# Performance work log

Hardware: AMD Instinct MI355X
Metric: run time of the kernel (lower is better)

Reference implementation:

```python
import jax, jax.numpy as jnp
import numpy as np

B, H, W, L, R = 8, 32, 32, 6, 384
NH = 6                      # num_heads
NE = L * R                  # n_embd = 2304
HID = 4 * NE                # tree-MLP hidden
M = sum(4 ** i for i in range(L))  # 1365 unique tree nodes
EPS = 1e-5


def build_node_id_map(h, w, l):
    # (h,w,level) -> unique node id; level k patches are 2^k x 2^k blocks
    ids = np.zeros((h, w, l), np.int32)
    off = 0
    for k in range(l):
        ws = w >> k
        hh = (np.arange(h) >> k)[:, None]
        ww = (np.arange(w) >> k)[None, :]
        ids[:, :, k] = off + hh * ws + ww
        off += (h >> k) * ws
    assert off == M
    return ids

_IDS = jnp.asarray(build_node_id_map(H, W, L).reshape(-1))  # (H*W*L,)


def layernorm(x, w, b):
    mu = jnp.mean(x, axis=-1, keepdims=True)
    var = jnp.mean(jnp.square(x - mu), axis=-1, keepdims=True)
    return (x - mu) * jax.lax.rsqrt(var + EPS) * w + b


def setup_inputs() -> dict:
    key = jax.random.key(0)
    ks = jax.random.split(key, 12)
    s = 0.02
    return {
        "x": jax.random.normal(ks[0], (B, H, W, L, R), jnp.float32),
        "ln1_w": jnp.ones((R,), jnp.float32), "ln1_b": jnp.zeros((R,), jnp.float32),
        "ln2_w": jnp.ones((R,), jnp.float32), "ln2_b": jnp.zeros((R,), jnp.float32),
        "wq": s * jax.random.normal(ks[1], (R, R), jnp.float32), "bq": jnp.zeros((R,), jnp.float32),
        "wk": s * jax.random.normal(ks[2], (R, R), jnp.float32), "bk": jnp.zeros((R,), jnp.float32),
        "wv": s * jax.random.normal(ks[3], (R, R), jnp.float32), "bv": jnp.zeros((R,), jnp.float32),
        "wo": s * jax.random.normal(ks[4], (R, R), jnp.float32), "bo": jnp.zeros((R,), jnp.float32),
        "w1": s * jax.random.normal(ks[5], (NE, HID), jnp.float32), "b1": jnp.zeros((HID,), jnp.float32),
        "w2": s * jax.random.normal(ks[6], (HID, NE), jnp.float32), "b2": jnp.zeros((NE,), jnp.float32),
    }


def reference(x, ln1_w, ln1_b, ln2_w, ln2_b, wq, bq, wk, bk, wv, bv, wo, bo, w1, b1, w2, b2):
    dh = R // NH
    # (1) LN per node
    x_ln = layernorm(x, ln1_w, ln1_b)
    # (2) unify duplicates -> (B, M, R) via segment mean over node ids
    xf = x_ln.reshape(B, H * W * L, R)
    counts = jnp.zeros((M,), x.dtype).at[_IDS].add(1.0)
    uniq = jnp.zeros((B, M, R), x.dtype).at[:, _IDS].add(xf) / counts[None, :, None]
    # (3) multi-head self-attention over the M unique tree nodes
    q = (uniq @ wq + bq).reshape(B, M, NH, dh)
    k = (uniq @ wk + bk).reshape(B, M, NH, dh)
    v = (uniq @ wv + bv).reshape(B, M, NH, dh)
    logits = jnp.einsum("bmhd,bnhd->bhmn", q, k) * (1.0 / jnp.sqrt(jnp.asarray(dh, x.dtype)))
    attn = jax.nn.softmax(logits, axis=-1)
    o = jnp.einsum("bhmn,bnhd->bmhd", attn, v).reshape(B, M, R)
    attn_out = o @ wo + bo
    # (4) scatter back to (B,H,W,L,R)
    x_attn = attn_out[:, _IDS].reshape(B, H, W, L, R)
    # (5) residual (dropout is identity in eval)
    x_res = x + x_attn
    # (6) LN -> tree MLP over full level stack at each (h,w)
    x_ln2 = layernorm(x_res, ln2_w, ln2_b)
    flat = x_ln2.reshape(B, H, W, NE)
    h1 = jax.nn.gelu(flat @ w1 + b1)
    mlp_out = (h1 @ w2 + b2).reshape(B, H, W, L, R)
    # (7) residual
    return x_res + mlp_out
```

## Files before the change

kernel.cpp:

```cpp
#include <hip/hip_runtime.h>
#include <cstddef>

#define B_    8
#define H_    32
#define W_    32
#define L_    6
#define R_    384
#define NH_   6
#define DH_   64
#define M_    1365
#define MPAD_ 1408
#define NE_   2304
#define HID_  9216
#define NROW_ 49152
#define BMR_  10920

typedef __bf16 bf16x8 __attribute__((ext_vector_type(8)));
typedef float  f32x4  __attribute__((ext_vector_type(4)));
typedef unsigned short us;

__device__ __forceinline__ unsigned short f2b(float f){
  unsigned u = __float_as_uint(f);
  u = (u + 0x7FFFu + ((u >> 16) & 1u)) >> 16;
  return (unsigned short)u;
}

__device__ __forceinline__ void gload16(const unsigned short* g, unsigned short* l){
  __builtin_amdgcn_global_load_lds(
      (const __attribute__((address_space(1))) unsigned int*)g,
      (__attribute__((address_space(3))) unsigned int*)l,
      16, 0, 0);
}

__device__ __forceinline__ float wsum(float s){
  #pragma unroll
  for (int o = 32; o > 0; o >>= 1) s += __shfl_xor(s, o, 64);
  return s;
}

__device__ __forceinline__ float rmax16(float v){
  v = fmaxf(v, __shfl_xor(v, 1, 64));
  v = fmaxf(v, __shfl_xor(v, 2, 64));
  v = fmaxf(v, __shfl_xor(v, 4, 64));
  v = fmaxf(v, __shfl_xor(v, 8, 64));
  return v;
}
__device__ __forceinline__ float rsum16(float v){
  v += __shfl_xor(v, 1, 64);
  v += __shfl_xor(v, 2, 64);
  v += __shfl_xor(v, 4, 64);
  v += __shfl_xor(v, 8, 64);
  return v;
}

__device__ __forceinline__ float gelu_fast(float x){
  float t = fmaf(0.07135482f * x, x * x, 1.5957691216f * x);
  return x / (1.0f + __expf(-t));
}

__global__ __launch_bounds__(256) void k_ln1_scatter(
    const float* __restrict__ x, const float* __restrict__ lw,
    const float* __restrict__ lb, float* __restrict__ uniq){
  int row  = blockIdx.x * 4 + (threadIdx.x >> 6);
  int lane = threadIdx.x & 63;
  int l  = row % 6;
  int hw = (row / 6) & 1023;
  int b  = row / 6144;
  int h = hw >> 5, w = hw & 31;
  const float* xr = x + (size_t)row * R_;
  float v[6]; float s = 0.f;
  #pragma unroll
  for (int i = 0; i < 6; i++){ v[i] = xr[lane + i*64]; s += v[i]; }
  s = wsum(s);
  float mu = s * (1.f/384.f);
  float qq = 0.f;
  #pragma unroll
  for (int i = 0; i < 6; i++){ float d = v[i]-mu; qq += d*d; }
  qq = wsum(qq);
  float rs = rsqrtf(qq * (1.f/384.f) + 1e-5f);
  int off = (4096 - (4096 >> (2*l))) / 3;
  int id  = off + (h >> l) * (32 >> l) + (w >> l);
  float invc = 1.f / (float)(1 << (2*l));
  float* ur = uniq + ((size_t)b * M_ + id) * R_;
  #pragma unroll
  for (int i = 0; i < 6; i++){
    int r = lane + i*64;
    float ln = (v[i]-mu)*rs*lw[r] + lb[r];
    atomicAdd(&ur[r], ln * invc);
  }
}

__global__ void k_cvt(const float* __restrict__ src, unsigned short* __restrict__ dst, int n){
  int i = blockIdx.x * 256 + threadIdx.x;
  if (i < n) dst[i] = f2b(src[i]);
}

__global__ void k_tcvt(const float* __restrict__ src, unsigned short* __restrict__ dst,
                       int K, int N){
  __shared__ float t[32][33];
  int n0 = blockIdx.x * 32, k0 = blockIdx.y * 32;
  int tx = threadIdx.x, ty = threadIdx.y;
  #pragma unroll
  for (int i = 0; i < 4; i++)
    t[ty + i*8][tx] = src[(size_t)(k0 + ty + i*8) * N + n0 + tx];
  __syncthreads();
  #pragma unroll
  for (int i = 0; i < 4; i++)
    dst[(size_t)(n0 + ty + i*8) * K + k0 + tx] = f2b(t[tx][ty + i*8]);
}

template<int EPI>
__global__ __launch_bounds__(256) void k_gemm(
    const unsigned short* __restrict__ A,
    const unsigned short* __restrict__ Bt,
    const float* __restrict__ bias,
    void* __restrict__ Cout,
    const float* __restrict__ res,
    void* __restrict__ aux1, void* __restrict__ aux2,
    int Mtot, int N, int K){
  __shared__ unsigned short As[128*64];
  __shared__ unsigned short Bs[128*64];
  int m0 = blockIdx.x * 128, n0 = blockIdx.y * 128;
  int tid  = threadIdx.x;
  int wv   = tid >> 6, lane = tid & 63;
  int quad = lane >> 4, l16 = lane & 15;
  int wm = (wv >> 1) * 64, wn = (wv & 1) * 64;
  int lr = lane >> 3;
  int lc = (lane & 7) * 8;
  f32x4 acc[4][4];
  #pragma unroll
  for (int a = 0; a < 4; a++)
    #pragma unroll
    for (int bidx = 0; bidx < 4; bidx++) acc[a][bidx] = 0.f;

  for (int k0 = 0; k0 < K; k0 += 64){
    #pragma unroll
    for (int j = 0; j < 4; j++){
      int c = wv*4 + j;
      int rowa = c*8 + lr;
      int gm = m0 + rowa; if (gm >= Mtot) gm = Mtot - 1;
      gload16(A + (size_t)gm * K + k0 + lc, &As[c*512]);
      int gn = n0 + rowa;
      gload16(Bt + (size_t)gn * K + k0 + lc, &Bs[c*512]);
    }
    asm volatile("s_waitcnt vmcnt(0)" ::: "memory");
    __syncthreads();
    #pragma unroll
    for (int ko = 0; ko < 2; ko++){
      bf16x8 af[4], bfr[4];
      #pragma unroll
      for (int t = 0; t < 4; t++){
        af[t]  = *(const bf16x8*)(&As[(wm + t*16 + l16)*64 + ko*32 + quad*8]);
        bfr[t] = *(const bf16x8*)(&Bs[(wn + t*16 + l16)*64 + ko*32 + quad*8]);
      }
      #pragma unroll
      for (int mt = 0; mt < 4; mt++)
        #pragma unroll
        for (int nt = 0; nt < 4; nt++)
          acc[mt][nt] = __builtin_amdgcn_mfma_f32_16x16x32_bf16(
              af[mt], bfr[nt], acc[mt][nt], 0, 0, 0);
    }
    __syncthreads();
  }
  #pragma unroll
  for (int mt = 0; mt < 4; mt++){
    #pragma unroll
    for (int i = 0; i < 4; i++){
      int row = m0 + wm + mt*16 + quad*4 + i;
      if (row >= Mtot) continue;
      #pragma unroll
      for (int nt = 0; nt < 4; nt++){
        int col = n0 + wn + nt*16 + l16;
        size_t idx = (size_t)row * N + col;
        float vv = acc[mt][nt][i] + bias[col];
        if (EPI == 5){
          int bb = row / M_;
          int mm = row - bb * M_;
          if (col < 384){
            ((unsigned short*)Cout)[(size_t)row * R_ + col] = f2b(vv);
          } else if (col < 768){
            ((unsigned short*)aux1)[(size_t)row * R_ + col - 384] = f2b(vv);
          } else {
            int c2 = col - 768;
            int hh = c2 >> 6, dd = c2 & 63;
            ((unsigned short*)aux2)[(((size_t)(bb*NH_ + hh))*DH_ + dd)*MPAD_ + mm] = f2b(vv);
          }
        } else {
          ((float*)Cout)[idx] = vv;
        }
      }
    }
  }
}


__device__ __forceinline__ void stage_half(const unsigned short* __restrict__ g,
                                           unsigned short* l, int K){
  int tid = threadIdx.x;
  int w  = tid >> 6;
  int ln = tid & 63;
  int rw = ln >> 3;
  int cs = ((ln & 7) ^ rw) * 8;
  gload16(g + (size_t)(w*16 + rw)     * K + cs, l + (w*16)*64);
  gload16(g + (size_t)(w*16 + 8 + rw) * K + cs, l + (w*16 + 8)*64);
}

__device__ __forceinline__ bf16x8 ldsfrag(const unsigned short* base, int row, int ko, int quad){
  int g = ((ko << 2) + quad) ^ (row & 7);
  return *(const bf16x8*)(base + row*64 + g*8);
}

#define SB0()  __builtin_amdgcn_sched_barrier(0)
#define MFMA16(A8, B8, C4) __builtin_amdgcn_mfma_f32_16x16x32_bf16(A8, B8, C4, 0, 0, 0)

#define PHASE(P, STAGE_STMT, TAIL_STMT)                                          \
  { bf16x8 aL0 = ldsfrag(curA, wr*128 + (2*(P))*16   + l16, 0, quad);            \
    bf16x8 aH0 = ldsfrag(curA, wr*128 + (2*(P))*16   + l16, 1, quad);            \
    bf16x8 aL1 = ldsfrag(curA, wr*128 + (2*(P)+1)*16 + l16, 0, quad);            \
    bf16x8 aH1 = ldsfrag(curA, wr*128 + (2*(P)+1)*16 + l16, 1, quad);            \
    STAGE_STMT;                                                                  \
    SB0();                                                                       \
    __builtin_amdgcn_s_barrier();                                                \
    asm volatile("s_waitcnt lgkmcnt(0)" ::: "memory");                           \
    SB0();                                                                       \
    __builtin_amdgcn_s_setprio(1);                                               \
    _Pragma("unroll")                                                            \
    for (int nt = 0; nt < 4; nt++)                                               \
      acc[2*(P)][nt]   = MFMA16(aL0, bfr[nt][0], acc[2*(P)][nt]);                \
    _Pragma("unroll")                                                            \
    for (int nt = 0; nt < 4; nt++)                                               \
      acc[2*(P)+1][nt] = MFMA16(aL1, bfr[nt][0], acc[2*(P)+1][nt]);              \
    _Pragma("unroll")                                                            \
    for (int nt = 0; nt < 4; nt++)                                               \
      acc[2*(P)][nt]   = MFMA16(aH0, bfr[nt][1], acc[2*(P)][nt]);                \
    _Pragma("unroll")                                                            \
    for (int nt = 0; nt < 4; nt++)                                               \
      acc[2*(P)+1][nt] = MFMA16(aH1, bfr[nt][1], acc[2*(P)+1][nt]);              \
    __builtin_amdgcn_s_setprio(0);                                               \
    TAIL_STMT;                                                                   \
    SB0();                                                                       \
    __builtin_amdgcn_s_barrier();                                                \
    SB0(); }

#define KTILE(CURBUF)                                                            \
  { us* curA = &lds8[CURBUF][0];                                                 \
    us* curB = curA + 16384;                                                     \
    us* nxtA = &lds8[(CURBUF) ^ 1][0];                                           \
    bool st1 = (t + 1 < NT), st2 = (t + 2 < NT);                                 \
    const us* An = Ab + (size_t)(t + 1) * 64;                                    \
    const us* Bn = Bb + (size_t)(t + 2) * 64;                                    \
    bf16x8 bfr[4][2];                                                            \
    _Pragma("unroll")                                                            \
    for (int nt = 0; nt < 4; nt++){                                              \
      bfr[nt][0] = ldsfrag(curB, wc*64 + nt*16 + l16, 0, quad);                  \
      bfr[nt][1] = ldsfrag(curB, wc*64 + nt*16 + l16, 1, quad);                  \
    }                                                                            \
    PHASE(0, { if (st1) stage_half(An,          nxtA,        Kfull); }, {});     \
    PHASE(1, { if (st1) stage_half(An + 128*KS, nxtA + 8192, Kfull); }, {});     \
    PHASE(2, { if (st2) stage_half(Bn,          curB,        Kfull); }, {});     \
    PHASE(3, { if (st2) stage_half(Bn + 128*KS, curB + 8192, Kfull); },          \
             { if (st1){                                                         \
                 if (st2) asm volatile("s_waitcnt vmcnt(4)" ::: "memory");       \
                 else     asm volatile("s_waitcnt vmcnt(0)" ::: "memory");       \
               } });                                                             \
    ++t; }

template<int EPI>
__global__ __launch_bounds__(512, 2) void k_gemm8(
    const unsigned short* __restrict__ A,
    const unsigned short* __restrict__ Bt,
    const float* __restrict__ bias,
    void* __restrict__ Cout,
    int Mtot, int N, int Kfull, int kLen){
  __shared__ unsigned short lds8[2][32768];

  int m0 = blockIdx.x * 256, n0 = blockIdx.y * 256;
  int k0 = blockIdx.z * kLen;
  int NT = kLen >> 6;
  const size_t KS = (size_t)Kfull;
  const us* Ab = A  + (size_t)m0 * KS + k0;
  const us* Bb = Bt + (size_t)n0 * KS + k0;
  int tid = threadIdx.x, wv = tid >> 6, lane = tid & 63;
  int quad = lane >> 4, l16 = lane & 15;
  int wr = wv >> 2, wc = wv & 3;

  f32x4 acc[8][4];
  #pragma unroll
  for (int a = 0; a < 8; a++)
    #pragma unroll
    for (int b = 0; b < 4; b++) acc[a][b] = 0.f;

  stage_half(Bb,               &lds8[0][16384],        Kfull);
  stage_half(Bb + 128*KS,      &lds8[0][16384 + 8192], Kfull);
  stage_half(Ab,               &lds8[0][0],            Kfull);
  stage_half(Ab + 128*KS,      &lds8[0][8192],         Kfull);
  if (NT > 1){
    stage_half(Bb + 64,             &lds8[1][16384],        Kfull);
    stage_half(Bb + 128*KS + 64,    &lds8[1][16384 + 8192], Kfull);
    asm volatile("s_waitcnt vmcnt(4)" ::: "memory");
  } else {
    asm volatile("s_waitcnt vmcnt(0)" ::: "memory");
  }
  __builtin_amdgcn_s_barrier();
  SB0();

  int t = 0;
  while (t < NT){
    KTILE(0);
    KTILE(1);
  }

  #pragma unroll
  for (int mt = 0; mt < 8; mt++){
    #pragma unroll
    for (int i = 0; i < 4; i++){
      int row = m0 + wr*128 + mt*16 + quad*4 + i;
      #pragma unroll
      for (int nt = 0; nt < 4; nt++){
        int col = n0 + wc*64 + nt*16 + l16;
        size_t idx = (size_t)row * N + col;
        float vv = acc[mt][nt][i];
        if (EPI == 1){
          ((unsigned short*)Cout)[idx] = f2b(gelu_fast(vv + bias[col]));
        } else {
          atomicAdd(&((float*)Cout)[idx], vv);
        }
      }
    }
  }
}

__global__ __launch_bounds__(256) void k_attn(
    const unsigned short* __restrict__ qb, const unsigned short* __restrict__ kb,
    const unsigned short* __restrict__ vtb, unsigned short* __restrict__ ob){
  __shared__ unsigned short Ks[64][64];
  __shared__ unsigned short Vt[64][64];
  __shared__ unsigned short Ps[4][16][64];
  int qt = blockIdx.x, bh = blockIdx.y;
  int b = bh / NH_, h = bh % NH_;
  int tid = threadIdx.x, wv = tid >> 6, lane = tid & 63;
  int quad = lane >> 4, l16 = lane & 15;

  int qm = qt*64 + wv*16 + l16;
  const unsigned short* qrow = qb + (size_t)(b*M_ + qm)*R_ + h*DH_;
  bf16x8 aq0 = *(const bf16x8*)(qrow + quad*8);
  bf16x8 aq1 = *(const bf16x8*)(qrow + 32 + quad*8);

  f32x4 oacc[4];
  #pragma unroll
  for (int db = 0; db < 4; db++) oacc[db] = 0.f;
  float mi[4], li[4];
  #pragma unroll
  for (int i = 0; i < 4; i++){ mi[i] = -1e30f; li[i] = 0.f; }

  for (int kt = 0; kt < 22; kt++){
    #pragma unroll
    for (int i = 0; i < 2; i++){
      int c = tid + i*256;
      int rowa = c >> 3, colc = (c & 7) * 8;
      *(uint4*)(&Ks[rowa][colc]) =
        *(const uint4*)(kb + (size_t)(b*M_ + kt*64 + rowa)*R_ + h*DH_ + colc);
      *(uint4*)(&Vt[rowa][colc]) =
        *(const uint4*)(vtb + ((size_t)bh*DH_ + rowa)*MPAD_ + kt*64 + colc);
    }
    __syncthreads();

    f32x4 s[4];
    #pragma unroll
    for (int nb = 0; nb < 4; nb++){
      s[nb] = 0.f;
      bf16x8 bk0 = *(const bf16x8*)(&Ks[nb*16 + l16][quad*8]);
      bf16x8 bk1 = *(const bf16x8*)(&Ks[nb*16 + l16][32 + quad*8]);
      s[nb] = __builtin_amdgcn_mfma_f32_16x16x32_bf16(aq0, bk0, s[nb], 0, 0, 0);
      s[nb] = __builtin_amdgcn_mfma_f32_16x16x32_bf16(aq1, bk1, s[nb], 0, 0, 0);
    }

    #pragma unroll
    for (int i = 0; i < 4; i++){
      float val[4];
      float mx = -1e30f;
      #pragma unroll
      for (int nb = 0; nb < 4; nb++){
        int gc = kt*64 + nb*16 + l16;
        val[nb] = (gc < M_) ? s[nb][i] * 0.125f : -1e30f;
        mx = fmaxf(mx, val[nb]);
      }
      mx = rmax16(mx);
      float mnew = fmaxf(mi[i], mx);
      float alpha = __expf(mi[i] - mnew);
      float rs = 0.f;
      #pragma unroll
      for (int nb = 0; nb < 4; nb++){
        float p = __expf(val[nb] - mnew);
        rs += p;
        Ps[wv][quad*4 + i][nb*16 + l16] = f2b(p);
      }
      rs = rsum16(rs);
      li[i] = li[i]*alpha + rs;
      mi[i] = mnew;
      #pragma unroll
      for (int db = 0; db < 4; db++) oacc[db][i] *= alpha;
    }

    #pragma unroll
    for (int ko = 0; ko < 2; ko++){
      bf16x8 ap = *(const bf16x8*)(&Ps[wv][l16][ko*32 + quad*8]);
      #pragma unroll
      for (int db = 0; db < 4; db++){
        bf16x8 bv = *(const bf16x8*)(&Vt[db*16 + l16][ko*32 + quad*8]);
        oacc[db] = __builtin_amdgcn_mfma_f32_16x16x32_bf16(ap, bv, oacc[db], 0, 0, 0);
      }
    }
    __syncthreads();
  }

  #pragma unroll
  for (int i = 0; i < 4; i++){
    int gm = qt*64 + wv*16 + quad*4 + i;
    if (gm < M_){
      float il = 1.f / li[i];
      #pragma unroll
      for (int db = 0; db < 4; db++)
        ob[(size_t)(b*M_ + gm)*R_ + h*DH_ + db*16 + l16] = f2b(oacc[db][i] * il);
    }
  }
}

__global__ __launch_bounds__(256) void k_scatter_ln2(
    const float* __restrict__ x, const float* __restrict__ attn,
    const float* __restrict__ lw, const float* __restrict__ lb,
    const float* __restrict__ b2,
    float* __restrict__ xres, unsigned short* __restrict__ flatb){
  int row  = blockIdx.x * 4 + (threadIdx.x >> 6);
  int lane = threadIdx.x & 63;
  int l  = row % 6;
  int hw = (row / 6) & 1023;
  int b  = row / 6144;
  int h = hw >> 5, w = hw & 31;
  int off = (4096 - (4096 >> (2*l))) / 3;
  int id  = off + (h >> l) * (32 >> l) + (w >> l);
  const float* ar = attn + ((size_t)b * M_ + id) * R_;
  const float* xr = x + (size_t)row * R_;
  float* orow = xres + (size_t)row * R_;
  float vv[6]; float s = 0.f;
  #pragma unroll
  for (int i = 0; i < 6; i++){
    int r = lane + i*64;
    float t = xr[r] + ar[r];
    vv[i] = t; s += t;
    orow[r] = t + b2[l*R_ + r];
  }
  s = wsum(s);
  float mu = s * (1.f/384.f);
  float qq = 0.f;
  #pragma unroll
  for (int i = 0; i < 6; i++){ float d = vv[i]-mu; qq += d*d; }
  qq = wsum(qq);
  float rs = rsqrtf(qq * (1.f/384.f) + 1e-5f);
  unsigned short* fr = flatb + (size_t)row * R_;
  #pragma unroll
  for (int i = 0; i < 6; i++){
    int r = lane + i*64;
    fr[r] = f2b((vv[i]-mu)*rs*lw[r] + lb[r]);
  }
}

extern "C" void kernel_launch(void* const* d_in, const int* in_sizes, int n_in,
                              void* d_out, int out_size, void* d_ws, size_t ws_size,
                              hipStream_t stream){
  const float* x    = (const float*)d_in[0];
  const float* ln1w = (const float*)d_in[1];
  const float* ln1b = (const float*)d_in[2];
  const float* ln2w = (const float*)d_in[3];
  const float* ln2b = (const float*)d_in[4];
  const float* wq   = (const float*)d_in[5];
  const float* bq   = (const float*)d_in[6];
  const float* wk   = (const float*)d_in[7];
  const float* bk   = (const float*)d_in[8];
  const float* wvv  = (const float*)d_in[9];
  const float* bv   = (const float*)d_in[10];
  const float* wo   = (const float*)d_in[11];
  const float* bo   = (const float*)d_in[12];
  const float* w1   = (const float*)d_in[13];
  const float* b1   = (const float*)d_in[14];
  const float* w2   = (const float*)d_in[15];
  const float* b2   = (const float*)d_in[16];
  float* out = (float*)d_out;

  char* ws = (char*)d_ws;
  unsigned short* h1b = (unsigned short*)ws;
  unsigned short* qb  = (unsigned short*)ws;
  unsigned short* kb  = qb + (size_t)BMR_ * R_;
  unsigned short* vtb = kb + (size_t)BMR_ * R_;
  unsigned short* ob  = vtb + (size_t)B_ * NH_ * DH_ * MPAD_;
  float* attn_o = (float*)(ob + (size_t)BMR_ * R_);
  size_t regA = ((size_t)8192 * HID_ * 2 + 255) & ~(size_t)255;
  char* p = ws + regA;
  float* uniqf = (float*)p;                   p += (size_t)BMR_ * R_ * 4;
  unsigned short* uniqb = (unsigned short*)p; p += (size_t)BMR_ * R_ * 2;
  unsigned short* wqkvt = (unsigned short*)p; p += (size_t)3 * R_ * R_ * 2;
  unsigned short* wot = (unsigned short*)p;   p += (size_t)R_ * R_ * 2;
  unsigned short* w1t = (unsigned short*)p;   p += (size_t)NE_ * HID_ * 2;
  unsigned short* w2t = (unsigned short*)p;   p += (size_t)NE_ * HID_ * 2;
  unsigned short* flatb = (unsigned short*)p; p += (size_t)NROW_ * R_ * 2;
  float* bqkv = (float*)p;                    p += (size_t)3 * R_ * 4;

  hipMemsetAsync(uniqf, 0, (size_t)BMR_ * R_ * 4, stream);
  hipMemsetAsync(vtb, 0, (size_t)B_ * NH_ * DH_ * MPAD_ * 2, stream);
  hipMemcpyAsync(bqkv,        bq, R_*4, hipMemcpyDeviceToDevice, stream);
  hipMemcpyAsync(bqkv + R_,   bk, R_*4, hipMemcpyDeviceToDevice, stream);
  hipMemcpyAsync(bqkv + 2*R_, bv, R_*4, hipMemcpyDeviceToDevice, stream);

  k_ln1_scatter<<<NROW_/4, 256, 0, stream>>>(x, ln1w, ln1b, uniqf);
  k_cvt<<<(BMR_*R_ + 255)/256, 256, 0, stream>>>(uniqf, uniqb, BMR_*R_);

  dim3 tb(32, 8);
  k_tcvt<<<dim3(R_/32, R_/32), tb, 0, stream>>>(wq, wqkvt, R_, R_);
  k_tcvt<<<dim3(R_/32, R_/32), tb, 0, stream>>>(wk, wqkvt + (size_t)R_*R_, R_, R_);
  k_tcvt<<<dim3(R_/32, R_/32), tb, 0, stream>>>(wvv, wqkvt + (size_t)2*R_*R_, R_, R_);
  k_tcvt<<<dim3(R_/32, R_/32), tb, 0, stream>>>(wo, wot, R_, R_);
  k_tcvt<<<dim3(HID_/32, NE_/32), tb, 0, stream>>>(w1, w1t, NE_, HID_);
  k_tcvt<<<dim3(NE_/32, HID_/32), tb, 0, stream>>>(w2, w2t, HID_, NE_);

  k_gemm<5><<<dim3(86, 9), 256, 0, stream>>>(uniqb, wqkvt, bqkv, qb, nullptr,
                                             kb, vtb, BMR_, 3*R_, R_);

  k_attn<<<dim3(22, 48), 256, 0, stream>>>(qb, kb, vtb, ob);

  k_gemm<0><<<dim3(86, 3), 256, 0, stream>>>(ob, wot, bo, attn_o, nullptr,
                                             nullptr, nullptr, BMR_, R_, R_);

  k_scatter_ln2<<<NROW_/4, 256, 0, stream>>>(x, attn_o, ln2w, ln2b, b2, out, flatb);

  k_gemm8<1><<<dim3(32, 36), 512, 0, stream>>>(flatb, w1t, b1, h1b,
                                               8192, HID_, NE_, NE_);
  k_gemm8<3><<<dim3(32, 9, 2), 512, 0, stream>>>(h1b, w2t, nullptr, out,
                                                 8192, NE_, HID_, HID_/2);
}
```

Before: 1.453 ms.

## Restructure GEMM k-tile schedule to double-buffer A fragments and cut barriers

Replaces the four barrier-separated phases per k-tile with a software-pipelined schedule. A-fragment LDS reads for the next row pair are issued while the current MFMA cluster runs, using partial lgkmcnt waits, and only two s_barriers are kept per tile instead of eight. Global-to-LDS staging of the next A and B tiles is grouped into two bursts. This targets barrier stalls and LDS-read latency at the cost of more live fragment registers and trickier synchronisation: the B staging into curB now depends on a single mid-tile barrier to avoid racing with other waves still reading it.

```diff
diff --git a/kernel.cpp b/kernel.cpp
--- a/kernel.cpp
+++ b/kernel.cpp
@@ -213,34 +213,28 @@
 #define SB0()  __builtin_amdgcn_sched_barrier(0)
 #define MFMA16(A8, B8, C4) __builtin_amdgcn_mfma_f32_16x16x32_bf16(A8, B8, C4, 0, 0, 0)
 
-#define PHASE(P, STAGE_STMT, TAIL_STMT)                                          \
-  { bf16x8 aL0 = ldsfrag(curA, wr*128 + (2*(P))*16   + l16, 0, quad);            \
-    bf16x8 aH0 = ldsfrag(curA, wr*128 + (2*(P))*16   + l16, 1, quad);            \
-    bf16x8 aL1 = ldsfrag(curA, wr*128 + (2*(P)+1)*16 + l16, 0, quad);            \
-    bf16x8 aH1 = ldsfrag(curA, wr*128 + (2*(P)+1)*16 + l16, 1, quad);            \
-    STAGE_STMT;                                                                  \
-    SB0();                                                                       \
-    __builtin_amdgcn_s_barrier();                                                \
-    asm volatile("s_waitcnt lgkmcnt(0)" ::: "memory");                           \
-    SB0();                                                                       \
-    __builtin_amdgcn_s_setprio(1);                                               \
+#define CL2(I0, AF)                                                              \
+  { __builtin_amdgcn_s_setprio(1);                                              \
     _Pragma("unroll")                                                            \
     for (int nt = 0; nt < 4; nt++)                                               \
-      acc[2*(P)][nt]   = MFMA16(aL0, bfr[nt][0], acc[2*(P)][nt]);                \
+      acc[I0][nt]   = MFMA16(AF[0][0], bfr[nt][0], acc[I0][nt]);                 \
     _Pragma("unroll")                                                            \
     for (int nt = 0; nt < 4; nt++)                                               \
-      acc[2*(P)+1][nt] = MFMA16(aL1, bfr[nt][0], acc[2*(P)+1][nt]);              \
+      acc[I0+1][nt] = MFMA16(AF[1][0], bfr[nt][0], acc[I0+1][nt]);               \
     _Pragma("unroll")                                                            \
     for (int nt = 0; nt < 4; nt++)                                               \
-      acc[2*(P)][nt]   = MFMA16(aH0, bfr[nt][1], acc[2*(P)][nt]);                \
+      acc[I0][nt]   = MFMA16(AF[0][1], bfr[nt][1], acc[I0][nt]);                 \
     _Pragma("unroll")                                                            \
     for (int nt = 0; nt < 4; nt++)                                               \
-      acc[2*(P)+1][nt] = MFMA16(aH1, bfr[nt][1], acc[2*(P)+1][nt]);              \
-    __builtin_amdgcn_s_setprio(0);                                               \
-    TAIL_STMT;                                                                   \
-    SB0();                                                                       \
-    __builtin_amdgcn_s_barrier();                                                \
-    SB0(); }
+      acc[I0+1][nt] = MFMA16(AF[1][1], bfr[nt][1], acc[I0+1][nt]);               \
+    __builtin_amdgcn_s_setprio(0); }
+
+#define RDA(DST, RBASE)                                                          \
+  _Pragma("unroll")                                                              \
+  for (int r = 0; r < 2; r++){                                                   \
+    DST[r][0] = ldsfrag(curA, wr*128 + ((RBASE)+r)*16 + l16, 0, quad);           \
+    DST[r][1] = ldsfrag(curA, wr*128 + ((RBASE)+r)*16 + l16, 1, quad);           \
+  }
 
 #define KTILE(CURBUF)                                                            \
   { us* curA = &lds8[CURBUF][0];                                                 \
@@ -249,20 +243,48 @@
     bool st1 = (t + 1 < NT), st2 = (t + 2 < NT);                                 \
     const us* An = Ab + (size_t)(t + 1) * 64;                                    \
     const us* Bn = Bb + (size_t)(t + 2) * 64;                                    \
-    bf16x8 bfr[4][2];                                                            \
+    bf16x8 bfr[4][2], a0[2][2], a1[2][2];                                        \
+        \
     _Pragma("unroll")                                                            \
     for (int nt = 0; nt < 4; nt++){                                              \
       bfr[nt][0] = ldsfrag(curB, wc*64 + nt*16 + l16, 0, quad);                  \
       bfr[nt][1] = ldsfrag(curB, wc*64 + nt*16 + l16, 1, quad);                  \
     }                                                                            \
-    PHASE(0, { if (st1) stage_half(An,          nxtA,        Kfull); }, {});     \
-    PHASE(1, { if (st1) stage_half(An + 128*KS, nxtA + 8192, Kfull); }, {});     \
-    PHASE(2, { if (st2) stage_half(Bn,          curB,        Kfull); }, {});     \
-    PHASE(3, { if (st2) stage_half(Bn + 128*KS, curB + 8192, Kfull); },          \
-             { if (st1){                                                         \
-                 if (st2) asm volatile("s_waitcnt vmcnt(4)" ::: "memory");       \
-                 else     asm volatile("s_waitcnt vmcnt(0)" ::: "memory");       \
-               } });                                                             \
+    SB0();                                                                       \
+    RDA(a0, 0); SB0();                                                           \
+    RDA(a1, 2); SB0();                                                           \
+    if (st1){ stage_half(An,          nxtA,        Kfull);                       \
+              stage_half(An + 128*KS, nxtA + 8192, Kfull); }                     \
+    SB0();                                                                       \
+    asm volatile("s_waitcnt lgkmcnt(4)" ::: "memory");    \
+    SB0();                                                                       \
+    CL2(0, a0);                                                                  \
+    SB0();                                                                       \
+    RDA(a0, 4); SB0();                                   \
+    asm volatile("s_waitcnt lgkmcnt(4)" ::: "memory");              \
+    SB0();                                                                       \
+    CL2(2, a1);                                                                  \
+    SB0();                                                                       \
+    __builtin_amdgcn_s_barrier();                      \
+    SB0();                                                                       \
+    if (st2){ stage_half(Bn,          curB,        Kfull);                       \
+              stage_half(Bn + 128*KS, curB + 8192, Kfull); }                     \
+    SB0();                                                                       \
+    RDA(a1, 6); SB0();                                   \
+    asm volatile("s_waitcnt lgkmcnt(4)" ::: "memory");        \
+    SB0();                                                                       \
+    CL2(4, a0);                                                                  \
+    SB0();                                                                       \
+    asm volatile("s_waitcnt lgkmcnt(0)" ::: "memory");        \
+    SB0();                                                                       \
+    CL2(6, a1);                                                                  \
+    SB0();                                                                       \
+    if (st1){                                                                    \
+      if (st2) asm volatile("s_waitcnt vmcnt(4)" ::: "memory");                  \
+      else     asm volatile("s_waitcnt vmcnt(0)" ::: "memory");                  \
+    }                                                                            \
+    __builtin_amdgcn_s_barrier();                                                \
+    SB0();                                                                       \
     ++t; }
 
 template<int EPI>
```

After: 1.420 ms. 1.02x faster.

## Replace 256x256 eight-wave MLP GEMM with 128x128 four-wave triple-buffer-style kernel

Applied to the files above, without the earlier changes.

The two large MLP GEMMs move from a 256x256 tile with 512 threads and a four-phase interleaved staging schedule to a 128x128 tile with 256 threads. Each K-step loads all fragments, barriers, issues the t+2 prefetch into the current buffer, runs 32 MFMAs, then waits. The smaller tile quadruples the grid and lowers LDS and registers per block, which helps occupancy and load balance. In exchange, arithmetic intensity per tile drops, global and L2 traffic roughly doubles, and the simpler schedule overlaps loads and compute less finely.

```diff
diff --git a/kernel.cpp b/kernel.cpp
--- a/kernel.cpp
+++ b/kernel.cpp
@@ -194,15 +194,16 @@
 }
 
 
-__device__ __forceinline__ void stage_half(const unsigned short* __restrict__ g,
-                                           unsigned short* l, int K){
+__device__ __forceinline__ void stage_tileO(const unsigned short* __restrict__ g,
+                                            unsigned short* l, int K){
   int tid = threadIdx.x;
   int w  = tid >> 6;
   int ln = tid & 63;
   int rw = ln >> 3;
   int cs = ((ln & 7) ^ rw) * 8;
-  gload16(g + (size_t)(w*16 + rw)     * K + cs, l + (w*16)*64);
-  gload16(g + (size_t)(w*16 + 8 + rw) * K + cs, l + (w*16 + 8)*64);
+  #pragma unroll
+  for (int k = 0; k < 4; k++)
+    gload16(g + (size_t)(w*32 + k*8 + rw) * K + cs, l + (w*32 + k*8)*64);
 }
 
 __device__ __forceinline__ bf16x8 ldsfrag(const unsigned short* base, int row, int ko, int quad){
@@ -213,91 +214,76 @@
 #define SB0()  __builtin_amdgcn_sched_barrier(0)
 #define MFMA16(A8, B8, C4) __builtin_amdgcn_mfma_f32_16x16x32_bf16(A8, B8, C4, 0, 0, 0)
 
-#define PHASE(P, STAGE_STMT, TAIL_STMT)                                          \
-  { bf16x8 aL0 = ldsfrag(curA, wr*128 + (2*(P))*16   + l16, 0, quad);            \
-    bf16x8 aH0 = ldsfrag(curA, wr*128 + (2*(P))*16   + l16, 1, quad);            \
-    bf16x8 aL1 = ldsfrag(curA, wr*128 + (2*(P)+1)*16 + l16, 0, quad);            \
-    bf16x8 aH1 = ldsfrag(curA, wr*128 + (2*(P)+1)*16 + l16, 1, quad);            \
-    STAGE_STMT;                                                                  \
-    SB0();                                                                       \
-    __builtin_amdgcn_s_barrier();                                                \
-    asm volatile("s_waitcnt lgkmcnt(0)" ::: "memory");                           \
-    SB0();                                                                       \
-    __builtin_amdgcn_s_setprio(1);                                               \
+#define KTILEO(CURBUF)                                                           \
+  { const us* curA = &ldsO[CURBUF][0];                                           \
+    const us* curB = curA + 8192;                                                \
+    bool st2 = (t + 2 < NT), st1 = (t + 1 < NT);                                 \
+    bf16x8 af[4][2], bfr[4][2];                                                  \
     _Pragma("unroll")                                                            \
-    for (int nt = 0; nt < 4; nt++)                                               \
-      acc[2*(P)][nt]   = MFMA16(aL0, bfr[nt][0], acc[2*(P)][nt]);                \
-    _Pragma("unroll")                                                            \
-    for (int nt = 0; nt < 4; nt++)                                               \
-      acc[2*(P)+1][nt] = MFMA16(aL1, bfr[nt][0], acc[2*(P)+1][nt]);              \
-    _Pragma("unroll")                                                            \
-    for (int nt = 0; nt < 4; nt++)                                               \
-      acc[2*(P)][nt]   = MFMA16(aH0, bfr[nt][1], acc[2*(P)][nt]);                \
-    _Pragma("unroll")                                                            \
-    for (int nt = 0; nt < 4; nt++)                                               \
-      acc[2*(P)+1][nt] = MFMA16(aH1, bfr[nt][1], acc[2*(P)+1][nt]);              \
-    __builtin_amdgcn_s_setprio(0);                                               \
-    TAIL_STMT;                                                                   \
-    SB0();                                                                       \
-    __builtin_amdgcn_s_barrier();                                                \
-    SB0(); }
-
-#define KTILE(CURBUF)                                                            \
-  { us* curA = &lds8[CURBUF][0];                                                 \
-    us* curB = curA + 16384;                                                     \
-    us* nxtA = &lds8[(CURBUF) ^ 1][0];                                           \
-    bool st1 = (t + 1 < NT), st2 = (t + 2 < NT);                                 \
-    const us* An = Ab + (size_t)(t + 1) * 64;                                    \
-    const us* Bn = Bb + (size_t)(t + 2) * 64;                                    \
-    bf16x8 bfr[4][2];                                                            \
+    for (int mt = 0; mt < 4; mt++){                                              \
+      af[mt][0] = ldsfrag(curA, wr*64 + mt*16 + l16, 0, quad);                   \
+      af[mt][1] = ldsfrag(curA, wr*64 + mt*16 + l16, 1, quad);                   \
+    }                                                                            \
     _Pragma("unroll")                                                            \
     for (int nt = 0; nt < 4; nt++){                                              \
       bfr[nt][0] = ldsfrag(curB, wc*64 + nt*16 + l16, 0, quad);                  \
       bfr[nt][1] = ldsfrag(curB, wc*64 + nt*16 + l16, 1, quad);                  \
     }                                                                            \
-    PHASE(0, { if (st1) stage_half(An,          nxtA,        Kfull); }, {});     \
-    PHASE(1, { if (st1) stage_half(An + 128*KS, nxtA + 8192, Kfull); }, {});     \
-    PHASE(2, { if (st2) stage_half(Bn,          curB,        Kfull); }, {});     \
-    PHASE(3, { if (st2) stage_half(Bn + 128*KS, curB + 8192, Kfull); },          \
-             { if (st1){                                                         \
-                 if (st2) asm volatile("s_waitcnt vmcnt(4)" ::: "memory");       \
-                 else     asm volatile("s_waitcnt vmcnt(0)" ::: "memory");       \
-               } });                                                             \
+    asm volatile("s_waitcnt lgkmcnt(0)" ::: "memory");                           \
+    SB0();                                                                       \
+    __builtin_amdgcn_s_barrier();              \
+    SB0();                                                                       \
+    if (st2){                                                                    \
+      stage_tileO(Ab + (size_t)(t + 2) * 64, &ldsO[CURBUF][0],    Kfull);        \
+      stage_tileO(Bb + (size_t)(t + 2) * 64, &ldsO[CURBUF][8192], Kfull);        \
+    }                                                                            \
+    SB0();                                                                       \
+    __builtin_amdgcn_s_setprio(1);                                               \
+    _Pragma("unroll")                                                            \
+    for (int ko = 0; ko < 2; ko++)                                               \
+      _Pragma("unroll")                                                          \
+      for (int mt = 0; mt < 4; mt++)                                             \
+        _Pragma("unroll")                                                        \
+        for (int nt = 0; nt < 4; nt++)                                           \
+          acc[mt][nt] = MFMA16(af[mt][ko], bfr[nt][ko], acc[mt][nt]);            \
+    __builtin_amdgcn_s_setprio(0);                                               \
+    SB0();                                                                       \
+    if (st2)      asm volatile("s_waitcnt vmcnt(8)" ::: "memory");               \
+    else if (st1) asm volatile("s_waitcnt vmcnt(0)" ::: "memory");               \
+    __builtin_amdgcn_s_barrier();                                                \
+    SB0();                                                                       \
     ++t; }
 
 template<int EPI>
-__global__ __launch_bounds__(512, 2) void k_gemm8(
+__global__ __launch_bounds__(256, 2) void k_gemmO(
     const unsigned short* __restrict__ A,
     const unsigned short* __restrict__ Bt,
     const float* __restrict__ bias,
     void* __restrict__ Cout,
     int Mtot, int N, int Kfull, int kLen){
-  __shared__ unsigned short lds8[2][32768];
-
-  int m0 = blockIdx.x * 256, n0 = blockIdx.y * 256;
+  __shared__ unsigned short ldsO[2][16384];
+
+  int m0 = blockIdx.x * 128, n0 = blockIdx.y * 128;
   int k0 = blockIdx.z * kLen;
   int NT = kLen >> 6;
-  const size_t KS = (size_t)Kfull;
-  const us* Ab = A  + (size_t)m0 * KS + k0;
-  const us* Bb = Bt + (size_t)n0 * KS + k0;
+  const us* Ab = A  + (size_t)m0 * (size_t)Kfull + k0;
+  const us* Bb = Bt + (size_t)n0 * (size_t)Kfull + k0;
   int tid = threadIdx.x, wv = tid >> 6, lane = tid & 63;
   int quad = lane >> 4, l16 = lane & 15;
-  int wr = wv >> 2, wc = wv & 3;
-
-  f32x4 acc[8][4];
-  #pragma unroll
-  for (int a = 0; a < 8; a++)
+  int wr = wv >> 1, wc = wv & 1;
+
+  f32x4 acc[4][4];
+  #pragma unroll
+  for (int a = 0; a < 4; a++)
     #pragma unroll
     for (int b = 0; b < 4; b++) acc[a][b] = 0.f;
 
-  stage_half(Bb,               &lds8[0][16384],        Kfull);
-  stage_half(Bb + 128*KS,      &lds8[0][16384 + 8192], Kfull);
-  stage_half(Ab,               &lds8[0][0],            Kfull);
-  stage_half(Ab + 128*KS,      &lds8[0][8192],         Kfull);
+  stage_tileO(Ab, &ldsO[0][0],    Kfull);
+  stage_tileO(Bb, &ldsO[0][8192], Kfull);
   if (NT > 1){
-    stage_half(Bb + 64,             &lds8[1][16384],        Kfull);
-    stage_half(Bb + 128*KS + 64,    &lds8[1][16384 + 8192], Kfull);
-    asm volatile("s_waitcnt vmcnt(4)" ::: "memory");
+    stage_tileO(Ab + 64, &ldsO[1][0],    Kfull);
+    stage_tileO(Bb + 64, &ldsO[1][8192], Kfull);
+    asm volatile("s_waitcnt vmcnt(8)" ::: "memory");
   } else {
     asm volatile("s_waitcnt vmcnt(0)" ::: "memory");
   }
@@ -306,15 +292,15 @@
 
   int t = 0;
   while (t < NT){
-    KTILE(0);
-    KTILE(1);
-  }
-
-  #pragma unroll
-  for (int mt = 0; mt < 8; mt++){
+    KTILEO(0);
+    KTILEO(1);
+  }
+
+  #pragma unroll
+  for (int mt = 0; mt < 4; mt++){
     #pragma unroll
     for (int i = 0; i < 4; i++){
-      int row = m0 + wr*128 + mt*16 + quad*4 + i;
+      int row = m0 + wr*64 + mt*16 + quad*4 + i;
       #pragma unroll
       for (int nt = 0; nt < 4; nt++){
         int col = n0 + wc*64 + nt*16 + l16;
@@ -532,8 +518,8 @@
 
   k_scatter_ln2<<<NROW_/4, 256, 0, stream>>>(x, attn_o, ln2w, ln2b, b2, out, flatb);
 
-  k_gemm8<1><<<dim3(32, 36), 512, 0, stream>>>(flatb, w1t, b1, h1b,
+  k_gemmO<1><<<dim3(64, 72), 256, 0, stream>>>(flatb, w1t, b1, h1b,
                                                8192, HID_, NE_, NE_);
-  k_gemm8<3><<<dim3(32, 9, 2), 512, 0, stream>>>(h1b, w2t, nullptr, out,
-                                                 8192, NE_, HID_, HID_/2);
-}
+  k_gemmO<3><<<dim3(64, 18, 2), 256, 0, stream>>>(h1b, w2t, nullptr, out,
+                                                  8192, NE_, HID_, HID_/2);
+}
```

New measurement: 1.404 ms. 3.4% less time.
